# Kernel optimization log

Measured on AMD Instinct MI355X. Metric: run time of the kernel, lower is better.

The kernel has to match this reference:

```python
import jax, jax.numpy as jnp
import numpy as np

N_SRC = 100000
N_DST = 50000
N_EDGES = 600000
D = 128


def setup_inputs() -> dict:
    key = jax.random.key(0)
    k1, k2, k3, k4, k5 = jax.random.split(key, 5)
    src_rep = jax.random.normal(k1, (N_SRC, D), dtype=jnp.float32)
    dst_rep = jax.random.normal(k2, (N_DST, D), dtype=jnp.float32)
    edge_src = jax.random.randint(k3, (N_EDGES,), 0, N_SRC, dtype=jnp.int64)
    edge_dst = jax.random.randint(k4, (N_EDGES,), 0, N_DST, dtype=jnp.int64)
    W = jax.random.normal(k5, (2 * D, D), dtype=jnp.float32) * (1.0 / np.sqrt(2 * D))
    b = jnp.zeros((D,), dtype=jnp.float32)
    return {"src_rep": src_rep, "dst_rep": dst_rep, "edge_src": edge_src,
            "edge_dst": edge_dst, "W": W, "b": b}


def reference(src_rep, dst_rep, edge_src, edge_dst, W, b):
    # copy_src: gather source reps along edges  [E, D]
    msgs = src_rep[edge_src]
    # sum reduce: scatter-add messages to destination nodes  [N_dst, D]
    agg = jax.ops.segment_sum(msgs, edge_dst, num_segments=dst_rep.shape[0])
    # NodeUpdater: concat(dst rep, summed messages) -> Linear -> activation
    # (Dropout is identity in eval mode.)
    concat = jnp.concatenate([dst_rep, agg], axis=1)  # [N_dst, 2D]
    new_rep = jax.nn.relu(concat @ W + b)  # [N_dst, D]
    return new_rep
```

## Files before the change

kernel.cpp:

```cpp
#include <hip/hip_runtime.h>

#define N_SRC   100000
#define N_DST   50000
#define N_EDGES 600000
#define D       128
#define RPB     16
#define PAD     48

#define CONV_BLOCKS  ((N_SRC * D / 4) / 256)
#define MISC_ELEMS   (2 * D * D + N_DST + D)
#define MISC_BLOCKS  ((MISC_ELEMS + 255) / 256)
#define FILL_BLOCKS  ((N_EDGES + 255) / 256)

typedef short bf16x8 __attribute__((ext_vector_type(8)));
typedef float f32x4  __attribute__((ext_vector_type(4)));

static __device__ __forceinline__ unsigned short f2bf(float f) {
    unsigned u = __float_as_uint(f);
    u += 0x7FFF + ((u >> 16) & 1);
    return (unsigned short)(u >> 16);
}
static __device__ __forceinline__ unsigned pk(float a, float b) {
    return (unsigned)f2bf(a) | ((unsigned)f2bf(b) << 16);
}
static __device__ __forceinline__ void addpk(float* a, uint4 u) {
    a[0] += __uint_as_float(u.x << 16);
    a[1] += __uint_as_float(u.x & 0xFFFF0000u);
    a[2] += __uint_as_float(u.y << 16);
    a[3] += __uint_as_float(u.y & 0xFFFF0000u);
    a[4] += __uint_as_float(u.z << 16);
    a[5] += __uint_as_float(u.z & 0xFFFF0000u);
    a[6] += __uint_as_float(u.w << 16);
    a[7] += __uint_as_float(u.w & 0xFFFF0000u);
}

__global__ __launch_bounds__(256) void prep_kernel(
    const float* __restrict__ src_rep, unsigned short* __restrict__ srcb,
    const float* __restrict__ W, unsigned short* __restrict__ Wt,
    int* __restrict__ cnt) {
    if (blockIdx.x < CONV_BLOCKS) {
        size_t t = (size_t)blockIdx.x * 256 + threadIdx.x;
        float4 v = reinterpret_cast<const float4*>(src_rep)[t];
        uint2 w;
        w.x = pk(v.x, v.y); w.y = pk(v.z, v.w);
        reinterpret_cast<uint2*>(srcb)[t] = w;
    } else {
        int t = (blockIdx.x - CONV_BLOCKS) * 256 + threadIdx.x;
        if (t < 2 * D * D) {
            int n = t >> 8, k = t & 255;
            Wt[n * 256 + k] = f2bf(W[(size_t)k * D + n]);
        }
        int c = t - 2 * D * D;
        if (c >= 0 && c < N_DST) cnt[c] = 0;
        int z = c - N_DST;
        if (z >= 0 && z < D) srcb[(size_t)N_SRC * D + z] = 0;
    }
}

__global__ __launch_bounds__(256) void fill_kernel(
    const int* __restrict__ edge_src, const int* __restrict__ edge_dst,
    int* __restrict__ cnt, int* __restrict__ perm) {
    int e = blockIdx.x * 256 + threadIdx.x;
    if (e < N_EDGES) {
        int d = edge_dst[e];
        int pos = atomicAdd(&cnt[d], 1);
        if (pos < PAD) perm[d * PAD + pos] = edge_src[e];
    }
}

__global__ __launch_bounds__(512) void fused_kernel(
    const unsigned short* __restrict__ srcb,
    const float* __restrict__ dst_rep,
    const int*   __restrict__ cnt,
    const int*   __restrict__ perm,
    const unsigned short* __restrict__ Wt,
    const float* __restrict__ bias,
    float*       __restrict__ out) {
    __shared__ __align__(16) unsigned short stage[8][2][1024];
    __shared__ unsigned short Abf[16 * 256];
    const int row0 = blockIdx.x * 16;
    const int tid = threadIdx.x, lane = tid & 63, wave = tid >> 6;
    const int q = lane >> 4, cl = lane & 15;

    const int dn0 = row0 + wave * 2;
    const int2 cc = *reinterpret_cast<const int2*>(&cnt[dn0]);
    const int dmA = min(cc.x, PAD) - 1, dmB = min(cc.y, PAD) - 1;
    const int dcA = max(dmA, 0), dcB = max(dmB, 0);
    const int piA = perm[(size_t)dn0 * PAD + min(lane, PAD - 1)];
    const int piB = perm[(size_t)(dn0 + 1) * PAD + min(lane, PAD - 1)];
    const int rounds = (max(dmA, dmB) + 8) >> 3;

    if (tid < 256) {
        int r = tid >> 4, b = tid & 15;
        const float4* p = reinterpret_cast<const float4*>(
            dst_rep + (size_t)(row0 + r) * D + b * 8);
        float4 v0 = p[0], v1 = p[1];
        uint4 w;
        w.x = pk(v0.x, v0.y); w.y = pk(v0.z, v0.w);
        w.z = pk(v1.x, v1.y); w.w = pk(v1.z, v1.w);
        *reinterpret_cast<uint4*>(&Abf[r * 256 + (b ^ (r & 7)) * 8]) = w;
    }

    unsigned short* stA = stage[wave][0];
    unsigned short* stB = stage[wave][1];
    float accA[8] = {}, accB[8] = {};
    for (int rd = 0; rd < rounds; ++rd) {
        const int base = rd * 8;
#pragma unroll
        for (int k = 0; k < 2; ++k) {
            int e = base + 4 * k + q;
            int rA = __shfl(piA, min(e, dcA)); rA = (e <= dmA) ? rA : N_SRC;
            int rB = __shfl(piB, min(e, dcB)); rB = (e <= dmB) ? rB : N_SRC;
            __builtin_amdgcn_global_load_lds(
                (const unsigned int*)(srcb + (size_t)rA * D + cl * 8),
                (unsigned int*)(stA + k * 512), 16, 0, 0);
            __builtin_amdgcn_global_load_lds(
                (const unsigned int*)(srcb + (size_t)rB * D + cl * 8),
                (unsigned int*)(stB + k * 512), 16, 0, 0);
        }
        asm volatile("s_waitcnt vmcnt(0)" ::: "memory");
        __builtin_amdgcn_sched_barrier(0);
#pragma unroll
        for (int k = 0; k < 2; ++k) {
            uint4 uA = *reinterpret_cast<const uint4*>(stA + k * 512 + q * 128 + cl * 8);
            uint4 uB = *reinterpret_cast<const uint4*>(stB + k * 512 + q * 128 + cl * 8);
            addpk(accA, uA); addpk(accB, uB);
        }
        asm volatile("s_waitcnt lgkmcnt(0)" ::: "memory");
        __builtin_amdgcn_sched_barrier(0);
    }

#pragma unroll
    for (int i = 0; i < 8; ++i) {
        accA[i] += __shfl_xor(accA[i], 16);
        accA[i] += __shfl_xor(accA[i], 32);
        accB[i] += __shfl_xor(accB[i], 16);
        accB[i] += __shfl_xor(accB[i], 32);
    }
    if (lane < 16) {
        const int rA = wave * 2, rB = wave * 2 + 1;
        uint4 w0, w1;
        w0.x = pk(accA[0], accA[1]); w0.y = pk(accA[2], accA[3]);
        w0.z = pk(accA[4], accA[5]); w0.w = pk(accA[6], accA[7]);
        w1.x = pk(accB[0], accB[1]); w1.y = pk(accB[2], accB[3]);
        w1.z = pk(accB[4], accB[5]); w1.w = pk(accB[6], accB[7]);
        *reinterpret_cast<uint4*>(&Abf[rA * 256 + ((16 + cl) ^ (rA & 7)) * 8]) = w0;
        *reinterpret_cast<uint4*>(&Abf[rB * 256 + ((16 + cl) ^ (rB & 7)) * 8]) = w1;
    }
    __syncthreads();

    f32x4 c0 = {0.f, 0.f, 0.f, 0.f};
    const int ar = lane & 15;
    const int kb = lane >> 4;
    const int n0 = wave * 16 + (lane & 15);
#pragma unroll
    for (int s = 0; s < 8; ++s) {
        int b = s * 4 + kb;
        bf16x8 af = *reinterpret_cast<const bf16x8*>(&Abf[ar * 256 + (b ^ (ar & 7)) * 8]);
        bf16x8 b0 = *reinterpret_cast<const bf16x8*>(&Wt[(size_t)n0 * 256 + s * 32 + kb * 8]);
        c0 = __builtin_amdgcn_mfma_f32_16x16x32_bf16(af, b0, c0, 0, 0, 0);
    }

    const float bv = bias[n0];
#pragma unroll
    for (int g = 0; g < 4; ++g) {
        size_t orow = row0 + (lane >> 4) * 4 + g;
        out[orow * D + n0] = fmaxf(c0[g] + bv, 0.f);
    }
}

__global__ __launch_bounds__(256) void prep_small_kernel(
    const float* __restrict__ W, unsigned short* __restrict__ Wt,
    int* __restrict__ cnt) {
    int t = blockIdx.x * 256 + threadIdx.x;
    if (t < 2 * D * D) {
        int n = t >> 8, k = t & 255;
        Wt[n * 256 + k] = f2bf(W[(size_t)k * D + n]);
    }
    int c = t - 2 * D * D;
    if (c >= 0 && c < N_DST) cnt[c] = 0;
}

__global__ __launch_bounds__(256) void gather_f32_kernel(
    const float* __restrict__ src_rep,
    const int*   __restrict__ cnt,
    const int*   __restrict__ perm,
    unsigned short* __restrict__ agg) {
    const int tid = threadIdx.x, lane = tid & 63, wave = tid >> 6;
    const int h = lane >> 5, c = lane & 31;
    const int dn = blockIdx.x * 4 + wave;
    const int deg = min(cnt[dn], PAD);
    const int pi = perm[(size_t)dn * PAD + min(lane, PAD - 1)];

    f32x4 a0 = {0.f, 0.f, 0.f, 0.f}, a1 = a0, a2 = a0, a3 = a0;
    const int dm1 = deg - 1;
    for (int base = 0; base < deg; base += 8) {
        int e0 = base + h, e1 = base + 2 + h, e2 = base + 4 + h, e3 = base + 6 + h;
        int s0 = __shfl(pi, min(e0, max(dm1, 0)));
        int s1 = __shfl(pi, min(e1, max(dm1, 0)));
        int s2 = __shfl(pi, min(e2, max(dm1, 0)));
        int s3 = __shfl(pi, min(e3, max(dm1, 0)));
        if (e0 <= dm1) a0 += *reinterpret_cast<const f32x4*>(src_rep + (size_t)s0 * D + c * 4);
        if (e1 <= dm1) a1 += *reinterpret_cast<const f32x4*>(src_rep + (size_t)s1 * D + c * 4);
        if (e2 <= dm1) a2 += *reinterpret_cast<const f32x4*>(src_rep + (size_t)s2 * D + c * 4);
        if (e3 <= dm1) a3 += *reinterpret_cast<const f32x4*>(src_rep + (size_t)s3 * D + c * 4);
    }
    a0 += a1; a2 += a3; a0 += a2;
#pragma unroll
    for (int qq = 0; qq < 4; ++qq) a0[qq] += __shfl_xor(a0[qq], 32);
    if (h == 0) {
        uint2 w;
        w.x = pk(a0[0], a0[1]); w.y = pk(a0[2], a0[3]);
        *reinterpret_cast<uint2*>(agg + (size_t)dn * D + c * 4) = w;
    }
}

__global__ __launch_bounds__(256) void gemm_kernel(
    const float* __restrict__ dst_rep,
    const unsigned short* __restrict__ agg,
    const unsigned short* __restrict__ Wt,
    const float* __restrict__ bias,
    float*       __restrict__ out) {
    __shared__ unsigned short Abf[RPB * 2 * D];
    const int row0 = blockIdx.x * RPB;
    const int tid = threadIdx.x, lane = tid & 63, wave = tid >> 6;
    {
        int r = tid >> 4, b = tid & 15;
        const float4* p = reinterpret_cast<const float4*>(
            dst_rep + (size_t)(row0 + r) * D + b * 8);
        float4 v0 = p[0], v1 = p[1];
        uint4 w;
        w.x = pk(v0.x, v0.y); w.y = pk(v0.z, v0.w);
        w.z = pk(v1.x, v1.y); w.w = pk(v1.z, v1.w);
        *reinterpret_cast<uint4*>(&Abf[r * 256 + (b ^ (r & 7)) * 8]) = w;
        uint4 g = *reinterpret_cast<const uint4*>(agg + (size_t)(row0 + r) * D + b * 8);
        *reinterpret_cast<uint4*>(&Abf[r * 256 + ((16 + b) ^ (r & 7)) * 8]) = g;
    }
    __syncthreads();

    f32x4 c0 = {0.f, 0.f, 0.f, 0.f}, c1 = {0.f, 0.f, 0.f, 0.f};
    const int ar = lane & 15;
    const int kb = lane >> 4;
    const int n0 = wave * 32 + (lane & 15);
#pragma unroll
    for (int s = 0; s < 8; ++s) {
        int b = s * 4 + kb;
        bf16x8 af = *reinterpret_cast<const bf16x8*>(&Abf[ar * 256 + (b ^ (ar & 7)) * 8]);
        int kbase = s * 32 + kb * 8;
        bf16x8 b0 = *reinterpret_cast<const bf16x8*>(&Wt[(size_t)n0 * 256 + kbase]);
        bf16x8 b1 = *reinterpret_cast<const bf16x8*>(&Wt[(size_t)(n0 + 16) * 256 + kbase]);
        c0 = __builtin_amdgcn_mfma_f32_16x16x32_bf16(af, b0, c0, 0, 0, 0);
        c1 = __builtin_amdgcn_mfma_f32_16x16x32_bf16(af, b1, c1, 0, 0, 0);
    }
    const float bv0 = bias[wave * 32 + (lane & 15)];
    const float bv1 = bias[wave * 32 + 16 + (lane & 15)];
#pragma unroll
    for (int g = 0; g < 4; ++g) {
        size_t orow = row0 + (lane >> 4) * 4 + g;
        out[orow * D + wave * 32 + (lane & 15)]      = fmaxf(c0[g] + bv0, 0.f);
        out[orow * D + wave * 32 + 16 + (lane & 15)] = fmaxf(c1[g] + bv1, 0.f);
    }
}

extern "C" void kernel_launch(void* const* d_in, const int* in_sizes, int n_in,
                              void* d_out, int out_size, void* d_ws, size_t ws_size,
                              hipStream_t stream) {
    const float* src_rep  = (const float*)d_in[0];
    const float* dst_rep  = (const float*)d_in[1];
    const int*   edge_src = (const int*)d_in[2];
    const int*   edge_dst = (const int*)d_in[3];
    const float* W        = (const float*)d_in[4];
    const float* bias     = (const float*)d_in[5];
    float*       out      = (float*)d_out;

    int* cnt  = (int*)d_ws;
    int* perm = cnt + N_DST;
    size_t wt_off = (((size_t)N_DST * (1 + PAD) * 4 + 255) / 256) * 256;
    unsigned short* Wt   = (unsigned short*)((char*)d_ws + wt_off);
    unsigned short* big  = Wt + (size_t)2 * D * D;
    const size_t need_full = wt_off + ((size_t)2 * D * D + (size_t)(N_SRC + 1) * D)
                             * sizeof(unsigned short);

    if (ws_size >= need_full) {
        unsigned short* srcb = big;
        prep_kernel<<<CONV_BLOCKS + MISC_BLOCKS, 256, 0, stream>>>(
            src_rep, srcb, W, Wt, cnt);
        fill_kernel<<<FILL_BLOCKS, 256, 0, stream>>>(edge_src, edge_dst, cnt, perm);
        fused_kernel<<<N_DST / 16, 512, 0, stream>>>(
            srcb, dst_rep, cnt, perm, Wt, bias, out);
    } else {
        unsigned short* agg = big;
        prep_small_kernel<<<MISC_BLOCKS, 256, 0, stream>>>(W, Wt, cnt);
        fill_kernel<<<FILL_BLOCKS, 256, 0, stream>>>(edge_src, edge_dst, cnt, perm);
        gather_f32_kernel<<<N_DST / 4, 256, 0, stream>>>(src_rep, cnt, perm, agg);
        gemm_kernel<<<N_DST / RPB, 256, 0, stream>>>(dst_rep, agg, Wt, bias, out);
    }
}
```

Baseline: 100.6 us.

## Double-buffer gather staging and process two edges per fill thread

The neighbor-row gather loop changes from batches of 8 edges per round with a full wait to a two-slot software pipeline of 4 edges per round. The next round's async global-to-LDS loads are issued before waiting on the current one, so gather latency overlaps the accumulation. Separately, the fill kernel now handles two edges per thread using int2 loads, which halves the thread count. Each round now carries fewer loads in flight, so overall memory-level parallelism may not improve.

```diff
diff --git a/kernel.cpp b/kernel.cpp
--- a/kernel.cpp
+++ b/kernel.cpp
@@ -10,7 +10,7 @@
 #define CONV_BLOCKS  ((N_SRC * D / 4) / 256)
 #define MISC_ELEMS   (2 * D * D + N_DST + D)
 #define MISC_BLOCKS  ((MISC_ELEMS + 255) / 256)
-#define FILL_BLOCKS  ((N_EDGES + 255) / 256)
+#define FILL_BLOCKS  ((N_EDGES / 2 + 255) / 256)
 
 typedef short bf16x8 __attribute__((ext_vector_type(8)));
 typedef float f32x4  __attribute__((ext_vector_type(4)));
@@ -60,11 +60,14 @@
 __global__ __launch_bounds__(256) void fill_kernel(
     const int* __restrict__ edge_src, const int* __restrict__ edge_dst,
     int* __restrict__ cnt, int* __restrict__ perm) {
-    int e = blockIdx.x * 256 + threadIdx.x;
-    if (e < N_EDGES) {
-        int d = edge_dst[e];
-        int pos = atomicAdd(&cnt[d], 1);
-        if (pos < PAD) perm[d * PAD + pos] = edge_src[e];
+    int e0 = (blockIdx.x * 256 + threadIdx.x) * 2;
+    if (e0 < N_EDGES) {
+        int2 s2 = *reinterpret_cast<const int2*>(edge_src + e0);
+        int2 d2 = *reinterpret_cast<const int2*>(edge_dst + e0);
+        int p0 = atomicAdd(&cnt[d2.x], 1);
+        if (p0 < PAD) perm[d2.x * PAD + p0] = s2.x;
+        int p1 = atomicAdd(&cnt[d2.y], 1);
+        if (p1 < PAD) perm[d2.y * PAD + p1] = s2.y;
     }
 }
 
@@ -76,7 +79,7 @@
     const unsigned short* __restrict__ Wt,
     const float* __restrict__ bias,
     float*       __restrict__ out) {
-    __shared__ __align__(16) unsigned short stage[8][2][1024];
+    __shared__ __align__(16) unsigned short stage[8][2][2][512];
     __shared__ unsigned short Abf[16 * 256];
     const int row0 = blockIdx.x * 16;
     const int tid = threadIdx.x, lane = tid & 63, wave = tid >> 6;
@@ -88,7 +91,7 @@
     const int dcA = max(dmA, 0), dcB = max(dmB, 0);
     const int piA = perm[(size_t)dn0 * PAD + min(lane, PAD - 1)];
     const int piB = perm[(size_t)(dn0 + 1) * PAD + min(lane, PAD - 1)];
-    const int rounds = (max(dmA, dmB) + 8) >> 3;
+    const int rounds = (max(dmA, dmB) + 4) >> 2;
 
     if (tid < 256) {
         int r = tid >> 4, b = tid & 15;
@@ -101,33 +104,37 @@
         *reinterpret_cast<uint4*>(&Abf[r * 256 + (b ^ (r & 7)) * 8]) = w;
     }
 
-    unsigned short* stA = stage[wave][0];
-    unsigned short* stB = stage[wave][1];
     float accA[8] = {}, accB[8] = {};
-    for (int rd = 0; rd < rounds; ++rd) {
-        const int base = rd * 8;
-#pragma unroll
-        for (int k = 0; k < 2; ++k) {
-            int e = base + 4 * k + q;
-            int rA = __shfl(piA, min(e, dcA)); rA = (e <= dmA) ? rA : N_SRC;
-            int rB = __shfl(piB, min(e, dcB)); rB = (e <= dmB) ? rB : N_SRC;
-            __builtin_amdgcn_global_load_lds(
-                (const unsigned int*)(srcb + (size_t)rA * D + cl * 8),
-                (unsigned int*)(stA + k * 512), 16, 0, 0);
-            __builtin_amdgcn_global_load_lds(
-                (const unsigned int*)(srcb + (size_t)rB * D + cl * 8),
-                (unsigned int*)(stB + k * 512), 16, 0, 0);
+    auto ISSUE = [&](int rd, int slot) {
+        int e = rd * 4 + q;
+        int rA = __shfl(piA, min(e, dcA)); rA = (e <= dmA) ? rA : N_SRC;
+        int rB = __shfl(piB, min(e, dcB)); rB = (e <= dmB) ? rB : N_SRC;
+        __builtin_amdgcn_global_load_lds(
+            (const unsigned int*)(srcb + (size_t)rA * D + cl * 8),
+            (unsigned int*)(&stage[wave][slot][0][0]), 16, 0, 0);
+        __builtin_amdgcn_global_load_lds(
+            (const unsigned int*)(srcb + (size_t)rB * D + cl * 8),
+            (unsigned int*)(&stage[wave][slot][1][0]), 16, 0, 0);
+    };
+    auto CONSUME = [&](int slot) {
+        uint4 uA = *reinterpret_cast<const uint4*>(&stage[wave][slot][0][q * 128 + cl * 8]);
+        uint4 uB = *reinterpret_cast<const uint4*>(&stage[wave][slot][1][q * 128 + cl * 8]);
+        addpk(accA, uA); addpk(accB, uB);
+    };
+
+    if (rounds > 0) {
+        ISSUE(0, 0);
+        for (int rd = 0; rd + 1 < rounds; ++rd) {
+            ISSUE(rd + 1, (rd + 1) & 1);
+            asm volatile("s_waitcnt vmcnt(2)" ::: "memory");
+            __builtin_amdgcn_sched_barrier(0);
+            CONSUME(rd & 1);
+            asm volatile("s_waitcnt lgkmcnt(0)" ::: "memory");
+            __builtin_amdgcn_sched_barrier(0);
         }
         asm volatile("s_waitcnt vmcnt(0)" ::: "memory");
         __builtin_amdgcn_sched_barrier(0);
-#pragma unroll
-        for (int k = 0; k < 2; ++k) {
-            uint4 uA = *reinterpret_cast<const uint4*>(stA + k * 512 + q * 128 + cl * 8);
-            uint4 uB = *reinterpret_cast<const uint4*>(stB + k * 512 + q * 128 + cl * 8);
-            addpk(accA, uA); addpk(accB, uB);
-        }
-        asm volatile("s_waitcnt lgkmcnt(0)" ::: "memory");
-        __builtin_amdgcn_sched_barrier(0);
+        CONSUME((rounds - 1) & 1);
     }
 
 #pragma unroll
```

New measurement: 98.53 us. -2.1%, faster.
